# Optimization experiments

Hardware: AMD Instinct MI355X
Metric: run time of the kernel (lower is better)

Reference implementation:

```python
import jax, jax.numpy as jnp
import numpy as np

RES = 16          # grid resolution per axis -> num_models = 4096
L_XYZ = 10        # xyz positional-encoding frequencies -> input_ch = 63
L_DIR = 4         # dir positional-encoding frequencies -> input_ch_views = 27
W = 32
N_RAYS, N_SAMPLES = 1024, 128
NM = RES * RES * RES


def _embed(x, L):
    # NeRF frequency encoding: [x, sin(2^k x), cos(2^k x)] for k in 0..L-1
    freqs = 2.0 ** jnp.arange(L, dtype=x.dtype)          # (L,)
    xf = x[..., None, :] * freqs[:, None]                # (N, L, 3)
    enc = jnp.concatenate([jnp.sin(xf), jnp.cos(xf)], axis=-1)
    return jnp.concatenate([x, enc.reshape(x.shape[0], -1)], axis=-1)


def setup_inputs() -> dict:
    key = jax.random.key(0)
    ks = jax.random.split(key, 16)
    s = 0.05
    pts = jax.random.uniform(ks[0], (N_RAYS, N_SAMPLES, 3), dtype=jnp.float32)
    vd = jax.random.normal(ks[1], (N_RAYS, 3), dtype=jnp.float32)
    vd = vd / jnp.linalg.norm(vd, axis=-1, keepdims=True)
    return {
        "pts": pts,
        "viewdirs": vd,
        "pts_w0": s * jax.random.normal(ks[2], (NM, W, 63), dtype=jnp.float32),
        "pts_b0": s * jax.random.normal(ks[3], (NM, W), dtype=jnp.float32),
        "pts_w1": s * jax.random.normal(ks[4], (NM, W, W), dtype=jnp.float32),
        "pts_b1": s * jax.random.normal(ks[5], (NM, W), dtype=jnp.float32),
        "feat_w": s * jax.random.normal(ks[6], (NM, W, W), dtype=jnp.float32),
        "feat_b": s * jax.random.normal(ks[7], (NM, W), dtype=jnp.float32),
        "sigma_w": s * jax.random.normal(ks[8], (NM, 1, W), dtype=jnp.float32),
        "sigma_b": s * jax.random.normal(ks[9], (NM, 1), dtype=jnp.float32),
        "view_w": s * jax.random.normal(ks[10], (NM, W, W + 27), dtype=jnp.float32),
        "view_b": s * jax.random.normal(ks[11], (NM, W), dtype=jnp.float32),
        "rgb_w": s * jax.random.normal(ks[12], (NM, 3, W), dtype=jnp.float32),
        "rgb_b": s * jax.random.normal(ks[13], (NM, 3), dtype=jnp.float32),
    }


def reference(pts, viewdirs, pts_w0, pts_b0, pts_w1, pts_b1, feat_w, feat_b,
              sigma_w, sigma_b, view_w, view_b, rgb_w, rgb_b):
    n_rays, n_samples, _ = pts.shape
    p = pts.reshape(-1, 3)                                        # (N, 3)
    v = jnp.broadcast_to(viewdirs[:, None, :],
                         (n_rays, n_samples, 3)).reshape(-1, 3)   # (N, 3)

    # voxel index (aabb = [0,1]^3)
    scaled = jnp.clip(p * RES, 0.0, RES - 1.0)
    i3 = scaled.astype(jnp.int32)
    idx = i3[:, 0] * (RES * RES) + i3[:, 1] * RES + i3[:, 2]      # (N,)

    ep = _embed(p, L_XYZ)                                         # (N, 63)
    ev = _embed(v, L_DIR)                                         # (N, 27)

    # per-point tiny MLP with gathered weights: h @ w^T + b
    h = jax.nn.relu(jnp.einsum('nd,nod->no', ep, pts_w0[idx]) + pts_b0[idx])
    h = jax.nn.relu(jnp.einsum('nd,nod->no', h, pts_w1[idx]) + pts_b1[idx])

    sigma = jnp.einsum('nd,nod->no', h, sigma_w[idx]) + sigma_b[idx]   # (N, 1)
    feat = jnp.einsum('nd,nod->no', h, feat_w[idx]) + feat_b[idx]      # (N, W)

    h2 = jnp.concatenate([feat, ev], axis=-1)                          # (N, W+27)
    h2 = jax.nn.relu(jnp.einsum('nd,nod->no', h2, view_w[idx]) + view_b[idx])
    rgb = jnp.einsum('nd,nod->no', h2, rgb_w[idx]) + rgb_b[idx]        # (N, 3)

    out = jnp.concatenate([rgb, sigma], axis=-1).reshape(n_rays, n_samples, 4)
    return out[..., :3], out[..., 3:4]
```

## Files before the change

kernel.cpp:

```cpp
#include <hip/hip_runtime.h>

#define NM    4096
#define NPTS  131072
#define CAP   128

typedef _Float16 h8 __attribute__((ext_vector_type(8)));
typedef _Float16 h2 __attribute__((ext_vector_type(2)));
typedef float    f4 __attribute__((ext_vector_type(4)));
typedef int      i4 __attribute__((ext_vector_type(4)));

#define MF(a, b, c) __builtin_amdgcn_mfma_f32_16x16x32_f16((a), (b), (c), 0, 0, 0)

#if __has_builtin(__builtin_amdgcn_global_load_lds)
#define USE_DMA 1
#else
#define USE_DMA 0
#endif

static __device__ inline h2 pk(float a, float b) {
    return __builtin_bit_cast(h2, __builtin_amdgcn_cvt_pkrtz(a, b));
}

static __device__ inline h8 pack8(float u0, float u1, float u2, float u3,
                                  float u4, float u5, float u6, float u7) {
    i4 t;
    t[0] = __builtin_bit_cast(int, pk(u0, u1));
    t[1] = __builtin_bit_cast(int, pk(u2, u3));
    t[2] = __builtin_bit_cast(int, pk(u4, u5));
    t[3] = __builtin_bit_cast(int, pk(u6, u7));
    return __builtin_bit_cast(h8, t);
}

static __device__ inline h8 lds_row8(const float* __restrict__ X, int base,
                                     int d0, int lim) {
    float u[8];
    #pragma unroll
    for (int jj = 0; jj < 8; jj++) {
        int d = d0 + jj;
        float raw = X[base + d];
        u[jj] = (d < lim) ? raw : 0.f;
    }
    return pack8(u[0], u[1], u[2], u[3], u[4], u[5], u[6], u[7]);
}

static __device__ inline h8 lds_row8a(const float* __restrict__ X, int off) {
    f4 v0 = *(const f4*)(X + off);
    f4 v1 = *(const f4*)(X + off + 4);
    return pack8(v0[0], v0[1], v0[2], v0[3], v1[0], v1[1], v1[2], v1[3]);
}

static __device__ inline h8 load_row8(const float* __restrict__ rb, int d0, int lim) {
    float u[8];
    #pragma unroll
    for (int jj = 0; jj < 8; jj++) {
        int d = d0 + jj;
        u[jj] = (d < lim) ? rb[d] : 0.f;
    }
    return pack8(u[0], u[1], u[2], u[3], u[4], u[5], u[6], u[7]);
}

static __device__ inline float encdim(int d, int lim, float x, float y, float z) {
    int tt = d - 3;
    int k  = tt / 6;
    int r  = tt - 6 * k;
    float p = x;
    p = (r == 1 || r == 4) ? y : p;
    p = (r == 2 || r == 5) ? z : p;
    float f   = __int_as_float((k + 127) << 23);
    float arg = p * f + ((r >= 3) ? 1.57079632679f : 0.f);
    float sv  = __sinf(arg);
    float raw = (d == 0) ? x : ((d == 1) ? y : z);
    float val = (d < 3) ? raw : sv;
    return (d < lim) ? val : 0.f;
}

static __device__ inline h8 makeB(f4 d0, f4 d1, int quad, int col) {
    int laneA = ((quad & 1) * 2) * 16 + col;
    int laneB = laneA + 16;
    float a0 = __shfl(d0[0], laneA), b0 = __shfl(d1[0], laneA);
    float a1 = __shfl(d0[1], laneA), b1 = __shfl(d1[1], laneA);
    float a2 = __shfl(d0[2], laneA), b2 = __shfl(d1[2], laneA);
    float a3 = __shfl(d0[3], laneA), b3 = __shfl(d1[3], laneA);
    float a4 = __shfl(d0[0], laneB), b4 = __shfl(d1[0], laneB);
    float a5 = __shfl(d0[1], laneB), b5 = __shfl(d1[1], laneB);
    float a6 = __shfl(d0[2], laneB), b6 = __shfl(d1[2], laneB);
    float a7 = __shfl(d0[3], laneB), b7 = __shfl(d1[3], laneB);
    bool hi = quad >= 2;
    return pack8(hi ? b0 : a0, hi ? b1 : a1, hi ? b2 : a2, hi ? b3 : a3,
                 hi ? b4 : a4, hi ? b5 : a5, hi ? b6 : a6, hi ? b7 : a7);
}

static __device__ inline f4 relu4(f4 a) {
    f4 r;
    r[0] = fmaxf(a[0], 0.f); r[1] = fmaxf(a[1], 0.f);
    r[2] = fmaxf(a[2], 0.f); r[3] = fmaxf(a[3], 0.f);
    return r;
}

#if USE_DMA
static __device__ inline void dma16(const float* g, const float* l) {
    __builtin_amdgcn_global_load_lds(
        (const __attribute__((address_space(1))) void*)g,
        (__attribute__((address_space(3))) void*)l, 16, 0, 0);
}
#endif

__global__ __launch_bounds__(256) void k_bucket(const float* __restrict__ pts,
                                                int* __restrict__ count,
                                                int* __restrict__ plist) {
    int n = blockIdx.x * 256 + threadIdx.x;
    if (n >= NPTS) return;
    float x = pts[3 * n + 0], y = pts[3 * n + 1], z = pts[3 * n + 2];
    int ix = (int)fminf(fmaxf(x * 16.f, 0.f), 15.f);
    int iy = (int)fminf(fmaxf(y * 16.f, 0.f), 15.f);
    int iz = (int)fminf(fmaxf(z * 16.f, 0.f), 15.f);
    int v = (ix << 8) | (iy << 4) | iz;
    int pos = atomicAdd(&count[v], 1);
    if (pos < CAP) plist[v * CAP + pos] = n;
}

__global__ __launch_bounds__(64) void k_mlp(
    const float* __restrict__ pts, const float* __restrict__ vds,
    const float* __restrict__ w0g, const float* __restrict__ b0g,
    const float* __restrict__ w1g, const float* __restrict__ b1g,
    const float* __restrict__ fwg, const float* __restrict__ fbg,
    const float* __restrict__ swg, const float* __restrict__ sbg,
    const float* __restrict__ vwg, const float* __restrict__ vbg,
    const float* __restrict__ rwg, const float* __restrict__ rbg,
    const int* __restrict__ count, const int* __restrict__ plist,
    float* __restrict__ out) {
    __shared__ __align__(16) float X[3040];

    const int lane = threadIdx.x & 63;
    const int col  = lane & 15;
    const int quad = lane >> 4;
    const int k8   = quad * 8;
    const int v    = blockIdx.x;
    const int c    = min(count[v], CAP);
    if (c == 0) return;

#if USE_DMA
    {
        const float* g = w0g + (size_t)v * 2016;
        #pragma unroll
        for (int k = 0; k < 7; k++) dma16(g + k * 256 + lane * 4, X + k * 256);
        if (lane < 56) dma16(g + 1792 + lane * 4, X + 1792);
        const float* g1 = w1g + (size_t)v * 1024;
        #pragma unroll
        for (int k = 0; k < 4; k++) dma16(g1 + k * 256 + lane * 4, X + 2016 + k * 256);
    }
#endif

    const int prow0 = plist[v * CAP + lane];
    const int prow1 = plist[v * CAP + 64 + lane];
    auto chunk_idx = [&](int base) -> int {
        int e = min(base + col, c - 1);
        int a = __shfl(prow0, e);
        int b = __shfl(prow1, e - 64);
        return (e < 64) ? a : b;
    };

    f4 cB0[2], cB1[2], cFB[2], cVB[2];
    #pragma unroll
    for (int Ti = 0; Ti < 2; Ti++) {
        int ro = v * 32 + Ti * 16 + quad * 4;
        cB0[Ti] = *(const f4*)(b0g + ro);
        cB1[Ti] = *(const f4*)(b1g + ro);
        cFB[Ti] = *(const f4*)(fbg + ro);
        cVB[Ti] = *(const f4*)(vbg + ro);
    }
    const float rb0 = rbg[v * 3 + 0], rb1 = rbg[v * 3 + 1], rb2 = rbg[v * 3 + 2];
    const float sb  = sbg[v];

    int ncur = chunk_idx(0);
    float px = pts[3 * ncur], py = pts[3 * ncur + 1], pz = pts[3 * ncur + 2];
    int ray = ncur >> 7;
    float dx = vds[3 * ray], dy = vds[3 * ray + 1], dz = vds[3 * ray + 2];

    int nnxt = 0;
    float qx = 0.f, qy = 0.f, qz = 0.f, ex = 0.f, ey = 0.f, ez = 0.f;
    if (16 < c) {
        nnxt = chunk_idx(16);
        qx = pts[3 * nnxt]; qy = pts[3 * nnxt + 1]; qz = pts[3 * nnxt + 2];
        int r2 = nnxt >> 7;
        ex = vds[3 * r2]; ey = vds[3 * r2 + 1]; ez = vds[3 * r2 + 2];
    }

    h8 bE0, bE1, bD;
    auto encode = [&](float sx, float sy, float sz, float tx, float ty, float tz) {
        bE0 = pack8(encdim(k8 + 0, 63, sx, sy, sz), encdim(k8 + 1, 63, sx, sy, sz),
                    encdim(k8 + 2, 63, sx, sy, sz), encdim(k8 + 3, 63, sx, sy, sz),
                    encdim(k8 + 4, 63, sx, sy, sz), encdim(k8 + 5, 63, sx, sy, sz),
                    encdim(k8 + 6, 63, sx, sy, sz), encdim(k8 + 7, 63, sx, sy, sz));
        bE1 = pack8(encdim(32 + k8 + 0, 63, sx, sy, sz), encdim(32 + k8 + 1, 63, sx, sy, sz),
                    encdim(32 + k8 + 2, 63, sx, sy, sz), encdim(32 + k8 + 3, 63, sx, sy, sz),
                    encdim(32 + k8 + 4, 63, sx, sy, sz), encdim(32 + k8 + 5, 63, sx, sy, sz),
                    encdim(32 + k8 + 6, 63, sx, sy, sz), encdim(32 + k8 + 7, 63, sx, sy, sz));
        bD  = pack8(encdim(k8 + 0, 27, tx, ty, tz), encdim(k8 + 1, 27, tx, ty, tz),
                    encdim(k8 + 2, 27, tx, ty, tz), encdim(k8 + 3, 27, tx, ty, tz),
                    encdim(k8 + 4, 27, tx, ty, tz), encdim(k8 + 5, 27, tx, ty, tz),
                    encdim(k8 + 6, 27, tx, ty, tz), encdim(k8 + 7, 27, tx, ty, tz));
    };
    encode(px, py, pz, dx, dy, dz);

    h8 aW0[2][2], aW1[2], aVW[2][2], aFW[2], aSG, aRGB;

#if USE_DMA
    asm volatile("s_waitcnt vmcnt(0)" ::: "memory");
    __builtin_amdgcn_sched_barrier(0);
    #pragma unroll
    for (int Ti = 0; Ti < 2; Ti++) {
        int r0 = (Ti * 16 + col) * 63;
        aW0[Ti][0] = lds_row8(X, r0, k8, 63);
        aW0[Ti][1] = lds_row8(X, r0, 32 + k8, 63);
        aW1[Ti] = lds_row8a(X, 2016 + (Ti * 16 + col) * 32 + k8);
    }
    asm volatile("s_waitcnt lgkmcnt(0)" ::: "memory");
    __builtin_amdgcn_sched_barrier(0);

    {
        const float* g = vwg + (size_t)v * 1888;
        #pragma unroll
        for (int k = 0; k < 7; k++) dma16(g + k * 256 + lane * 4, X + k * 256);
        if (lane < 24) dma16(g + 1792 + lane * 4, X + 1792);
        const float* g1 = fwg + (size_t)v * 1024;
        #pragma unroll
        for (int k = 0; k < 4; k++) dma16(g1 + k * 256 + lane * 4, X + 1888 + k * 256);
        if (lane < 8)  dma16(swg + (size_t)v * 32 + lane * 4, X + 2912);
        if (lane < 24) dma16(rwg + (size_t)v * 96 + lane * 4, X + 2944);
    }
#else
    {
        #pragma unroll
        for (int Ti = 0; Ti < 2; Ti++) {
            const float* rb = w0g + (size_t)v * 2016 + (Ti * 16 + col) * 63;
            aW0[Ti][0] = load_row8(rb, k8, 63);
            aW0[Ti][1] = load_row8(rb, 32 + k8, 63);
            aW1[Ti] = load_row8(w1g + (size_t)v * 1024 + (Ti * 16 + col) * 32, k8, 32);
        }
    }
#endif

    const f4 z4 = {0.f, 0.f, 0.f, 0.f};

    f4 d0 = MF(aW0[0][0], bE0, cB0[0]); d0 = MF(aW0[0][1], bE1, d0);
    f4 d1 = MF(aW0[1][0], bE0, cB0[1]); d1 = MF(aW0[1][1], bE1, d1);
    d0 = relu4(d0); d1 = relu4(d1);
    h8 bH = makeB(d0, d1, quad, col);
    f4 e0 = MF(aW1[0], bH, cB1[0]);
    f4 e1 = MF(aW1[1], bH, cB1[1]);
    e0 = relu4(e0); e1 = relu4(e1);
    h8 bG = makeB(e0, e1, quad, col);

#if USE_DMA
    asm volatile("s_waitcnt vmcnt(0)" ::: "memory");
    __builtin_amdgcn_sched_barrier(0);
    #pragma unroll
    for (int Ti = 0; Ti < 2; Ti++) {
        int r1 = (Ti * 16 + col) * 59;
        aVW[Ti][0] = lds_row8(X, r1, k8, 59);
        aVW[Ti][1] = lds_row8(X, r1, 32 + k8, 59);
        aFW[Ti] = lds_row8a(X, 1888 + (Ti * 16 + col) * 32 + k8);
    }
    aSG  = (col == 0) ? lds_row8a(X, 2912 + k8) : h8{};
    aRGB = (col < 3) ? lds_row8a(X, 2944 + col * 32 + k8) : h8{};
#else
    {
        #pragma unroll
        for (int Ti = 0; Ti < 2; Ti++) {
            const float* rb = vwg + (size_t)v * 1888 + (Ti * 16 + col) * 59;
            aVW[Ti][0] = load_row8(rb, k8, 59);
            aVW[Ti][1] = load_row8(rb, 32 + k8, 59);
            aFW[Ti] = load_row8(fwg + (size_t)v * 1024 + (Ti * 16 + col) * 32, k8, 32);
        }
        aSG  = (col == 0) ? load_row8(swg + (size_t)v * 32, k8, 32) : h8{};
        aRGB = (col < 3) ? load_row8(rwg + (size_t)v * 96 + col * 32, k8, 32) : h8{};
    }
#endif

    {
        f4 s  = MF(aSG, bG, z4);
        f4 f0 = MF(aFW[0], bG, cFB[0]);
        f4 f1 = MF(aFW[1], bG, cFB[1]);
        h8 bF = makeB(f0, f1, quad, col);
        f4 v0 = MF(aVW[0][0], bF, cVB[0]); v0 = MF(aVW[0][1], bD, v0);
        f4 v1 = MF(aVW[1][0], bF, cVB[1]); v1 = MF(aVW[1][1], bD, v1);
        v0 = relu4(v0); v1 = relu4(v1);
        h8 bV = makeB(v0, v1, quad, col);
        f4 o  = MF(aRGB, bV, z4);
        if (quad == 0 && col < c) {
            out[3 * ncur + 0] = o[0] + rb0;
            out[3 * ncur + 1] = o[1] + rb1;
            out[3 * ncur + 2] = o[2] + rb2;
            out[3 * NPTS + ncur] = s[0] + sb;
        }
    }

    for (int base = 16; base < c; base += 16) {
        const int n = nnxt;
        const float cx = qx, cy = qy, cz = qz;
        const float fx = ex, fy = ey, fz = ez;

        if (base + 16 < c) {
            nnxt = chunk_idx(base + 16);
            qx = pts[3 * nnxt]; qy = pts[3 * nnxt + 1]; qz = pts[3 * nnxt + 2];
            int r2 = nnxt >> 7;
            ex = vds[3 * r2]; ey = vds[3 * r2 + 1]; ez = vds[3 * r2 + 2];
        }

        encode(cx, cy, cz, fx, fy, fz);

        d0 = MF(aW0[0][0], bE0, cB0[0]); d0 = MF(aW0[0][1], bE1, d0);
        d1 = MF(aW0[1][0], bE0, cB0[1]); d1 = MF(aW0[1][1], bE1, d1);
        d0 = relu4(d0); d1 = relu4(d1);
        bH = makeB(d0, d1, quad, col);

        e0 = MF(aW1[0], bH, cB1[0]);
        e1 = MF(aW1[1], bH, cB1[1]);
        e0 = relu4(e0); e1 = relu4(e1);
        bG = makeB(e0, e1, quad, col);

        f4 s  = MF(aSG, bG, z4);
        f4 f0 = MF(aFW[0], bG, cFB[0]);
        f4 f1 = MF(aFW[1], bG, cFB[1]);
        h8 bF = makeB(f0, f1, quad, col);

        f4 v0 = MF(aVW[0][0], bF, cVB[0]); v0 = MF(aVW[0][1], bD, v0);
        f4 v1 = MF(aVW[1][0], bF, cVB[1]); v1 = MF(aVW[1][1], bD, v1);
        v0 = relu4(v0); v1 = relu4(v1);
        h8 bV = makeB(v0, v1, quad, col);
        f4 o  = MF(aRGB, bV, z4);

        if (quad == 0 && (base + col) < c) {
            out[3 * n + 0] = o[0] + rb0;
            out[3 * n + 1] = o[1] + rb1;
            out[3 * n + 2] = o[2] + rb2;
            out[3 * NPTS + n] = s[0] + sb;
        }
    }
}

extern "C" void kernel_launch(void* const* d_in, const int* in_sizes, int n_in,
                              void* d_out, int out_size, void* d_ws, size_t ws_size,
                              hipStream_t stream) {
    const float* pts = (const float*)d_in[0];
    const float* vds = (const float*)d_in[1];
    const float* w0  = (const float*)d_in[2];
    const float* b0  = (const float*)d_in[3];
    const float* w1  = (const float*)d_in[4];
    const float* b1  = (const float*)d_in[5];
    const float* fw  = (const float*)d_in[6];
    const float* fb  = (const float*)d_in[7];
    const float* sw  = (const float*)d_in[8];
    const float* sb  = (const float*)d_in[9];
    const float* vw  = (const float*)d_in[10];
    const float* vb  = (const float*)d_in[11];
    const float* rw  = (const float*)d_in[12];
    const float* rb  = (const float*)d_in[13];
    float* out = (float*)d_out;

    int* count = (int*)d_ws;
    int* plist = (int*)((char*)d_ws + NM * sizeof(int));

    (void)hipMemsetAsync(count, 0, NM * sizeof(int), stream);
    k_bucket<<<NPTS / 256, 256, 0, stream>>>(pts, count, plist);
    k_mlp<<<NM, 64, 0, stream>>>(pts, vds, w0, b0, w1, b1, fw, fb, sw, sb,
                                 vw, vb, rw, rb, count, plist, out);
}
```

Measured before the change: 165.3 us.

## Process four voxels per block with double-buffered LDS weight prefetch

```diff
diff --git a/kernel.cpp b/kernel.cpp
--- a/kernel.cpp
+++ b/kernel.cpp
@@ -3,6 +3,8 @@
 #define NM    4096
 #define NPTS  131072
 #define CAP   128
+#define NV    4
+#define NBLK  (NM / NV)
 
 typedef _Float16 h8 __attribute__((ext_vector_type(8)));
 typedef _Float16 h2 __attribute__((ext_vector_type(2)));
@@ -129,64 +131,78 @@
     const float* __restrict__ rwg, const float* __restrict__ rbg,
     const int* __restrict__ count, const int* __restrict__ plist,
     float* __restrict__ out) {
-    __shared__ __align__(16) float X[3040];
+    __shared__ __align__(16) float X[2][3040];
 
     const int lane = threadIdx.x & 63;
     const int col  = lane & 15;
     const int quad = lane >> 4;
     const int k8   = quad * 8;
-    const int v    = blockIdx.x;
-    const int c    = min(count[v], CAP);
-    if (c == 0) return;
-
-#if USE_DMA
-    {
+    const int vbase = blockIdx.x * NV;
+
+#if USE_DMA
+    auto dmaA = [&](int v, float* Xb) {
         const float* g = w0g + (size_t)v * 2016;
         #pragma unroll
-        for (int k = 0; k < 7; k++) dma16(g + k * 256 + lane * 4, X + k * 256);
-        if (lane < 56) dma16(g + 1792 + lane * 4, X + 1792);
+        for (int k = 0; k < 7; k++) dma16(g + k * 256 + lane * 4, Xb + k * 256);
+        if (lane < 56) dma16(g + 1792 + lane * 4, Xb + 1792);
         const float* g1 = w1g + (size_t)v * 1024;
         #pragma unroll
-        for (int k = 0; k < 4; k++) dma16(g1 + k * 256 + lane * 4, X + 2016 + k * 256);
-    }
-#endif
-
-    const int prow0 = plist[v * CAP + lane];
-    const int prow1 = plist[v * CAP + 64 + lane];
-    auto chunk_idx = [&](int base) -> int {
-        int e = min(base + col, c - 1);
-        int a = __shfl(prow0, e);
-        int b = __shfl(prow1, e - 64);
-        return (e < 64) ? a : b;
+        for (int k = 0; k < 4; k++) dma16(g1 + k * 256 + lane * 4, Xb + 2016 + k * 256);
     };
-
-    f4 cB0[2], cB1[2], cFB[2], cVB[2];
-    #pragma unroll
-    for (int Ti = 0; Ti < 2; Ti++) {
-        int ro = v * 32 + Ti * 16 + quad * 4;
-        cB0[Ti] = *(const f4*)(b0g + ro);
-        cB1[Ti] = *(const f4*)(b1g + ro);
-        cFB[Ti] = *(const f4*)(fbg + ro);
-        cVB[Ti] = *(const f4*)(vbg + ro);
-    }
-    const float rb0 = rbg[v * 3 + 0], rb1 = rbg[v * 3 + 1], rb2 = rbg[v * 3 + 2];
-    const float sb  = sbg[v];
-
-    int ncur = chunk_idx(0);
-    float px = pts[3 * ncur], py = pts[3 * ncur + 1], pz = pts[3 * ncur + 2];
-    int ray = ncur >> 7;
-    float dx = vds[3 * ray], dy = vds[3 * ray + 1], dz = vds[3 * ray + 2];
-
-    int nnxt = 0;
-    float qx = 0.f, qy = 0.f, qz = 0.f, ex = 0.f, ey = 0.f, ez = 0.f;
-    if (16 < c) {
-        nnxt = chunk_idx(16);
-        qx = pts[3 * nnxt]; qy = pts[3 * nnxt + 1]; qz = pts[3 * nnxt + 2];
-        int r2 = nnxt >> 7;
-        ex = vds[3 * r2]; ey = vds[3 * r2 + 1]; ez = vds[3 * r2 + 2];
-    }
-
+    auto dmaB = [&](int v, float* Xb) {
+        const float* g = vwg + (size_t)v * 1888;
+        #pragma unroll
+        for (int k = 0; k < 7; k++) dma16(g + k * 256 + lane * 4, Xb + k * 256);
+        if (lane < 24) dma16(g + 1792 + lane * 4, Xb + 1792);
+        const float* g1 = fwg + (size_t)v * 1024;
+        #pragma unroll
+        for (int k = 0; k < 4; k++) dma16(g1 + k * 256 + lane * 4, Xb + 1888 + k * 256);
+        if (lane < 8)  dma16(swg + (size_t)v * 32 + lane * 4, Xb + 2912);
+        if (lane < 24) dma16(rwg + (size_t)v * 96 + lane * 4, Xb + 2944);
+    };
+#endif
+
+    int c_n = 0, prow0_n = 0, prow1_n = 0;
+    f4 cB0_n[2], cB1_n[2], cFB_n[2], cVB_n[2];
+    float rb0_n = 0.f, rb1_n = 0.f, rb2_n = 0.f, sb_n = 0.f;
+    int n0_n = 0;
+    float px_n = 0.f, py_n = 0.f, pz_n = 0.f, dx_n = 0.f, dy_n = 0.f, dz_n = 0.f;
+
+    auto pf_meta = [&](int v) {
+        c_n = min(count[v], CAP);
+        prow0_n = plist[v * CAP + lane];
+        prow1_n = plist[v * CAP + 64 + lane];
+        #pragma unroll
+        for (int Ti = 0; Ti < 2; Ti++) {
+            int ro = v * 32 + Ti * 16 + quad * 4;
+            cB0_n[Ti] = *(const f4*)(b0g + ro);
+            cB1_n[Ti] = *(const f4*)(b1g + ro);
+            cFB_n[Ti] = *(const f4*)(fbg + ro);
+            cVB_n[Ti] = *(const f4*)(vbg + ro);
+        }
+        rb0_n = rbg[v * 3 + 0]; rb1_n = rbg[v * 3 + 1]; rb2_n = rbg[v * 3 + 2];
+        sb_n  = sbg[v];
+    };
+    auto pf_pts = [&]() {
+        if (c_n > 0) {
+            int e = min(col, c_n - 1);
+            n0_n = __shfl(prow0_n, e);
+            px_n = pts[3 * n0_n]; py_n = pts[3 * n0_n + 1]; pz_n = pts[3 * n0_n + 2];
+            int ray = n0_n >> 7;
+            dx_n = vds[3 * ray]; dy_n = vds[3 * ray + 1]; dz_n = vds[3 * ray + 2];
+        }
+    };
+
+    pf_meta(vbase);
+#if USE_DMA
+    dmaA(vbase, X[0]);
+#endif
+    pf_pts();
+
+    h8 aW0[2][2], aW1[2], aVW[2][2], aFW[2], aSG, aRGB;
     h8 bE0, bE1, bD;
+    const f4 z4 = {0.f, 0.f, 0.f, 0.f};
+
     auto encode = [&](float sx, float sy, float sz, float tx, float ty, float tz) {
         bE0 = pack8(encdim(k8 + 0, 63, sx, sy, sz), encdim(k8 + 1, 63, sx, sy, sz),
                     encdim(k8 + 2, 63, sx, sy, sz), encdim(k8 + 3, 63, sx, sy, sz),
@@ -201,142 +217,182 @@
                     encdim(k8 + 4, 27, tx, ty, tz), encdim(k8 + 5, 27, tx, ty, tz),
                     encdim(k8 + 6, 27, tx, ty, tz), encdim(k8 + 7, 27, tx, ty, tz));
     };
-    encode(px, py, pz, dx, dy, dz);
-
-    h8 aW0[2][2], aW1[2], aVW[2][2], aFW[2], aSG, aRGB;
-
-#if USE_DMA
-    asm volatile("s_waitcnt vmcnt(0)" ::: "memory");
-    __builtin_amdgcn_sched_barrier(0);
-    #pragma unroll
-    for (int Ti = 0; Ti < 2; Ti++) {
-        int r0 = (Ti * 16 + col) * 63;
-        aW0[Ti][0] = lds_row8(X, r0, k8, 63);
-        aW0[Ti][1] = lds_row8(X, r0, 32 + k8, 63);
-        aW1[Ti] = lds_row8a(X, 2016 + (Ti * 16 + col) * 32 + k8);
-    }
-    asm volatile("s_waitcnt lgkmcnt(0)" ::: "memory");
-    __builtin_amdgcn_sched_barrier(0);
-
-    {
-        const float* g = vwg + (size_t)v * 1888;
-        #pragma unroll
-        for (int k = 0; k < 7; k++) dma16(g + k * 256 + lane * 4, X + k * 256);
-        if (lane < 24) dma16(g + 1792 + lane * 4, X + 1792);
-        const float* g1 = fwg + (size_t)v * 1024;
-        #pragma unroll
-        for (int k = 0; k < 4; k++) dma16(g1 + k * 256 + lane * 4, X + 1888 + k * 256);
-        if (lane < 8)  dma16(swg + (size_t)v * 32 + lane * 4, X + 2912);
-        if (lane < 24) dma16(rwg + (size_t)v * 96 + lane * 4, X + 2944);
-    }
+
+    int cur = 0;
+    for (int iv = 0; iv < NV; iv++) {
+        float* Xb = X[cur];
+        const int v = vbase + iv;
+
+        const int c = c_n;
+        const int prow0 = prow0_n, prow1 = prow1_n;
+        f4 cB0[2] = {cB0_n[0], cB0_n[1]}, cB1[2] = {cB1_n[0], cB1_n[1]};
+        f4 cFB[2] = {cFB_n[0], cFB_n[1]}, cVB[2] = {cVB_n[0], cVB_n[1]};
+        const float rb0 = rb0_n, rb1 = rb1_n, rb2 = rb2_n, sb = sb_n;
+        const int n0 = n0_n;
+        const float px = px_n, py = py_n, pz = pz_n;
+        const float dx = dx_n, dy = dy_n, dz = dz_n;
+        const bool hasW = c > 0;
+
+        auto chunk_idx = [&](int base) -> int {
+            int e = min(base + col, c - 1);
+            int a = __shfl(prow0, e);
+            int b = __shfl(prow1, e - 64);
+            return (e < 64) ? a : b;
+        };
+
+#if USE_DMA
+        asm volatile("s_waitcnt vmcnt(0)" ::: "memory");
+        __builtin_amdgcn_sched_barrier(0);
+
+        if (hasW) {
+            #pragma unroll
+            for (int Ti = 0; Ti < 2; Ti++) {
+                int r0 = (Ti * 16 + col) * 63;
+                aW0[Ti][0] = lds_row8(Xb, r0, k8, 63);
+                aW0[Ti][1] = lds_row8(Xb, r0, 32 + k8, 63);
+                aW1[Ti] = lds_row8a(Xb, 2016 + (Ti * 16 + col) * 32 + k8);
+            }
+        }
 #else
-    {
-        #pragma unroll
-        for (int Ti = 0; Ti < 2; Ti++) {
-            const float* rb = w0g + (size_t)v * 2016 + (Ti * 16 + col) * 63;
-            aW0[Ti][0] = load_row8(rb, k8, 63);
-            aW0[Ti][1] = load_row8(rb, 32 + k8, 63);
-            aW1[Ti] = load_row8(w1g + (size_t)v * 1024 + (Ti * 16 + col) * 32, k8, 32);
-        }
-    }
-#endif
-
-    const f4 z4 = {0.f, 0.f, 0.f, 0.f};
-
-    f4 d0 = MF(aW0[0][0], bE0, cB0[0]); d0 = MF(aW0[0][1], bE1, d0);
-    f4 d1 = MF(aW0[1][0], bE0, cB0[1]); d1 = MF(aW0[1][1], bE1, d1);
-    d0 = relu4(d0); d1 = relu4(d1);
-    h8 bH = makeB(d0, d1, quad, col);
-    f4 e0 = MF(aW1[0], bH, cB1[0]);
-    f4 e1 = MF(aW1[1], bH, cB1[1]);
-    e0 = relu4(e0); e1 = relu4(e1);
-    h8 bG = makeB(e0, e1, quad, col);
-
-#if USE_DMA
-    asm volatile("s_waitcnt vmcnt(0)" ::: "memory");
-    __builtin_amdgcn_sched_barrier(0);
-    #pragma unroll
-    for (int Ti = 0; Ti < 2; Ti++) {
-        int r1 = (Ti * 16 + col) * 59;
-        aVW[Ti][0] = lds_row8(X, r1, k8, 59);
-        aVW[Ti][1] = lds_row8(X, r1, 32 + k8, 59);
-        aFW[Ti] = lds_row8a(X, 1888 + (Ti * 16 + col) * 32 + k8);
-    }
-    aSG  = (col == 0) ? lds_row8a(X, 2912 + k8) : h8{};
-    aRGB = (col < 3) ? lds_row8a(X, 2944 + col * 32 + k8) : h8{};
+        if (hasW) {
+            #pragma unroll
+            for (int Ti = 0; Ti < 2; Ti++) {
+                const float* rb = w0g + (size_t)v * 2016 + (Ti * 16 + col) * 63;
+                aW0[Ti][0] = load_row8(rb, k8, 63);
+                aW0[Ti][1] = load_row8(rb, 32 + k8, 63);
+                aW1[Ti] = load_row8(w1g + (size_t)v * 1024 + (Ti * 16 + col) * 32, k8, 32);
+            }
+        }
+#endif
+
+        int n1 = 0;
+        float qx = 0.f, qy = 0.f, qz = 0.f, ex = 0.f, ey = 0.f, ez = 0.f;
+        if (c > 16) {
+            n1 = chunk_idx(16);
+            qx = pts[3 * n1]; qy = pts[3 * n1 + 1]; qz = pts[3 * n1 + 2];
+            int r2 = n1 >> 7;
+            ex = vds[3 * r2]; ey = vds[3 * r2 + 1]; ez = vds[3 * r2 + 2];
+        }
+
+        if (iv + 1 < NV) pf_meta(v + 1);
+
+#if USE_DMA
+        asm volatile("s_waitcnt lgkmcnt(0)" ::: "memory");
+        __builtin_amdgcn_sched_barrier(0);
+        dmaB(v, Xb);
+#endif
+
+        f4 d0, d1, e0, e1;
+        h8 bH, bG;
+        if (hasW) {
+            encode(px, py, pz, dx, dy, dz);
+            d0 = MF(aW0[0][0], bE0, cB0[0]); d0 = MF(aW0[0][1], bE1, d0);
+            d1 = MF(aW0[1][0], bE0, cB0[1]); d1 = MF(aW0[1][1], bE1, d1);
+            d0 = relu4(d0); d1 = relu4(d1);
+            bH = makeB(d0, d1, quad, col);
+            e0 = MF(aW1[0], bH, cB1[0]);
+            e1 = MF(aW1[1], bH, cB1[1]);
+            e0 = relu4(e0); e1 = relu4(e1);
+            bG = makeB(e0, e1, quad, col);
+        }
+
+#if USE_DMA
+        __builtin_amdgcn_sched_barrier(0);
+        asm volatile("s_waitcnt vmcnt(0)" ::: "memory");
+        __builtin_amdgcn_sched_barrier(0);
+
+        if (hasW) {
+            #pragma unroll
+            for (int Ti = 0; Ti < 2; Ti++) {
+                int r1 = (Ti * 16 + col) * 59;
+                aVW[Ti][0] = lds_row8(Xb, r1, k8, 59);
+                aVW[Ti][1] = lds_row8(Xb, r1, 32 + k8, 59);
+                aFW[Ti] = lds_row8a(Xb, 1888 + (Ti * 16 + col) * 32 + k8);
+            }
+            aSG  = (col == 0) ? lds_row8a(Xb, 2912 + k8) : h8{};
+            aRGB = (col < 3) ? lds_row8a(Xb, 2944 + col * 32 + k8) : h8{};
+        }
 #else
-    {
-        #pragma unroll
-        for (int Ti = 0; Ti < 2; Ti++) {
-            const float* rb = vwg + (size_t)v * 1888 + (Ti * 16 + col) * 59;
-            aVW[Ti][0] = load_row8(rb, k8, 59);
-            aVW[Ti][1] = load_row8(rb, 32 + k8, 59);
-            aFW[Ti] = load_row8(fwg + (size_t)v * 1024 + (Ti * 16 + col) * 32, k8, 32);
-        }
-        aSG  = (col == 0) ? load_row8(swg + (size_t)v * 32, k8, 32) : h8{};
-        aRGB = (col < 3) ? load_row8(rwg + (size_t)v * 96 + col * 32, k8, 32) : h8{};
-    }
-#endif
-
-    {
-        f4 s  = MF(aSG, bG, z4);
-        f4 f0 = MF(aFW[0], bG, cFB[0]);
-        f4 f1 = MF(aFW[1], bG, cFB[1]);
-        h8 bF = makeB(f0, f1, quad, col);
-        f4 v0 = MF(aVW[0][0], bF, cVB[0]); v0 = MF(aVW[0][1], bD, v0);
-        f4 v1 = MF(aVW[1][0], bF, cVB[1]); v1 = MF(aVW[1][1], bD, v1);
-        v0 = relu4(v0); v1 = relu4(v1);
-        h8 bV = makeB(v0, v1, quad, col);
-        f4 o  = MF(aRGB, bV, z4);
-        if (quad == 0 && col < c) {
-            out[3 * ncur + 0] = o[0] + rb0;
-            out[3 * ncur + 1] = o[1] + rb1;
-            out[3 * ncur + 2] = o[2] + rb2;
-            out[3 * NPTS + ncur] = s[0] + sb;
-        }
-    }
-
-    for (int base = 16; base < c; base += 16) {
-        const int n = nnxt;
-        const float cx = qx, cy = qy, cz = qz;
-        const float fx = ex, fy = ey, fz = ez;
-
-        if (base + 16 < c) {
-            nnxt = chunk_idx(base + 16);
-            qx = pts[3 * nnxt]; qy = pts[3 * nnxt + 1]; qz = pts[3 * nnxt + 2];
-            int r2 = nnxt >> 7;
-            ex = vds[3 * r2]; ey = vds[3 * r2 + 1]; ez = vds[3 * r2 + 2];
-        }
-
-        encode(cx, cy, cz, fx, fy, fz);
-
-        d0 = MF(aW0[0][0], bE0, cB0[0]); d0 = MF(aW0[0][1], bE1, d0);
-        d1 = MF(aW0[1][0], bE0, cB0[1]); d1 = MF(aW0[1][1], bE1, d1);
-        d0 = relu4(d0); d1 = relu4(d1);
-        bH = makeB(d0, d1, quad, col);
-
-        e0 = MF(aW1[0], bH, cB1[0]);
-        e1 = MF(aW1[1], bH, cB1[1]);
-        e0 = relu4(e0); e1 = relu4(e1);
-        bG = makeB(e0, e1, quad, col);
-
-        f4 s  = MF(aSG, bG, z4);
-        f4 f0 = MF(aFW[0], bG, cFB[0]);
-        f4 f1 = MF(aFW[1], bG, cFB[1]);
-        h8 bF = makeB(f0, f1, quad, col);
-
-        f4 v0 = MF(aVW[0][0], bF, cVB[0]); v0 = MF(aVW[0][1], bD, v0);
-        f4 v1 = MF(aVW[1][0], bF, cVB[1]); v1 = MF(aVW[1][1], bD, v1);
-        v0 = relu4(v0); v1 = relu4(v1);
-        h8 bV = makeB(v0, v1, quad, col);
-        f4 o  = MF(aRGB, bV, z4);
-
-        if (quad == 0 && (base + col) < c) {
-            out[3 * n + 0] = o[0] + rb0;
-            out[3 * n + 1] = o[1] + rb1;
-            out[3 * n + 2] = o[2] + rb2;
-            out[3 * NPTS + n] = s[0] + sb;
-        }
+        if (hasW) {
+            #pragma unroll
+            for (int Ti = 0; Ti < 2; Ti++) {
+                const float* rb = vwg + (size_t)v * 1888 + (Ti * 16 + col) * 59;
+                aVW[Ti][0] = load_row8(rb, k8, 59);
+                aVW[Ti][1] = load_row8(rb, 32 + k8, 59);
+                aFW[Ti] = load_row8(fwg + (size_t)v * 1024 + (Ti * 16 + col) * 32, k8, 32);
+            }
+            aSG  = (col == 0) ? load_row8(swg + (size_t)v * 32, k8, 32) : h8{};
+            aRGB = (col < 3) ? load_row8(rwg + (size_t)v * 96 + col * 32, k8, 32) : h8{};
+        }
+#endif
+
+        if (iv + 1 < NV) {
+            pf_pts();
+#if USE_DMA
+            dmaA(v + 1, X[cur ^ 1]);
+#endif
+        }
+
+        if (hasW) {
+            {
+                f4 s  = MF(aSG, bG, z4);
+                f4 f0 = MF(aFW[0], bG, cFB[0]);
+                f4 f1 = MF(aFW[1], bG, cFB[1]);
+                h8 bF = makeB(f0, f1, quad, col);
+                f4 v0 = MF(aVW[0][0], bF, cVB[0]); v0 = MF(aVW[0][1], bD, v0);
+                f4 v1 = MF(aVW[1][0], bF, cVB[1]); v1 = MF(aVW[1][1], bD, v1);
+                v0 = relu4(v0); v1 = relu4(v1);
+                h8 bV = makeB(v0, v1, quad, col);
+                f4 o  = MF(aRGB, bV, z4);
+                if (quad == 0 && col < c) {
+                    out[3 * n0 + 0] = o[0] + rb0;
+                    out[3 * n0 + 1] = o[1] + rb1;
+                    out[3 * n0 + 2] = o[2] + rb2;
+                    out[3 * NPTS + n0] = s[0] + sb;
+                }
+            }
+
+            auto do_chunk = [&](int n, bool active) {
+                d0 = MF(aW0[0][0], bE0, cB0[0]); d0 = MF(aW0[0][1], bE1, d0);
+                d1 = MF(aW0[1][0], bE0, cB0[1]); d1 = MF(aW0[1][1], bE1, d1);
+                d0 = relu4(d0); d1 = relu4(d1);
+                bH = makeB(d0, d1, quad, col);
+                e0 = MF(aW1[0], bH, cB1[0]);
+                e1 = MF(aW1[1], bH, cB1[1]);
+                e0 = relu4(e0); e1 = relu4(e1);
+                bG = makeB(e0, e1, quad, col);
+                f4 s  = MF(aSG, bG, z4);
+                f4 f0 = MF(aFW[0], bG, cFB[0]);
+                f4 f1 = MF(aFW[1], bG, cFB[1]);
+                h8 bF = makeB(f0, f1, quad, col);
+                f4 v0 = MF(aVW[0][0], bF, cVB[0]); v0 = MF(aVW[0][1], bD, v0);
+                f4 v1 = MF(aVW[1][0], bF, cVB[1]); v1 = MF(aVW[1][1], bD, v1);
+                v0 = relu4(v0); v1 = relu4(v1);
+                h8 bV = makeB(v0, v1, quad, col);
+                f4 o  = MF(aRGB, bV, z4);
+                if (quad == 0 && active) {
+                    out[3 * n + 0] = o[0] + rb0;
+                    out[3 * n + 1] = o[1] + rb1;
+                    out[3 * n + 2] = o[2] + rb2;
+                    out[3 * NPTS + n] = s[0] + sb;
+                }
+            };
+
+            if (c > 16) {
+                encode(qx, qy, qz, ex, ey, ez);
+                do_chunk(n1, (16 + col) < c);
+            }
+            for (int base = 32; base < c; base += 16) {
+                int n = chunk_idx(base);
+                float gx = pts[3 * n], gy = pts[3 * n + 1], gz = pts[3 * n + 2];
+                int r3 = n >> 7;
+                float hx = vds[3 * r3], hy = vds[3 * r3 + 1], hz = vds[3 * r3 + 2];
+                encode(gx, gy, gz, hx, hy, hz);
+                do_chunk(n, (base + col) < c);
+            }
+        }
+
+        cur ^= 1;
     }
 }
 
@@ -364,6 +420,6 @@
 
     (void)hipMemsetAsync(count, 0, NM * sizeof(int), stream);
     k_bucket<<<NPTS / 256, 256, 0, stream>>>(pts, count, plist);
-    k_mlp<<<NM, 64, 0, stream>>>(pts, vds, w0, b0, w1, b1, fw, fb, sw, sb,
-                                 vw, vb, rw, rb, count, plist, out);
-}
+    k_mlp<<<NBLK, 64, 0, stream>>>(pts, vds, w0, b0, w1, b1, fw, fb, sw, sb,
+                                   vw, vb, rw, rb, count, plist, out);
+}
```

Measured after the change: 170.0 us. 1.03x slower.

## Replace LDS DMA staging with direct vectorized global weight loads into registers

Applied to the files above, without the earlier changes.

```diff
diff --git a/kernel.cpp b/kernel.cpp
--- a/kernel.cpp
+++ b/kernel.cpp
@@ -8,14 +8,9 @@
 typedef _Float16 h2 __attribute__((ext_vector_type(2)));
 typedef float    f4 __attribute__((ext_vector_type(4)));
 typedef int      i4 __attribute__((ext_vector_type(4)));
+typedef float    f4u __attribute__((ext_vector_type(4), aligned(4)));
 
 #define MF(a, b, c) __builtin_amdgcn_mfma_f32_16x16x32_f16((a), (b), (c), 0, 0, 0)
-
-#if __has_builtin(__builtin_amdgcn_global_load_lds)
-#define USE_DMA 1
-#else
-#define USE_DMA 0
-#endif
 
 static __device__ inline h2 pk(float a, float b) {
     return __builtin_bit_cast(h2, __builtin_amdgcn_cvt_pkrtz(a, b));
@@ -29,34 +24,6 @@
     t[2] = __builtin_bit_cast(int, pk(u4, u5));
     t[3] = __builtin_bit_cast(int, pk(u6, u7));
     return __builtin_bit_cast(h8, t);
-}
-
-static __device__ inline h8 lds_row8(const float* __restrict__ X, int base,
-                                     int d0, int lim) {
-    float u[8];
-    #pragma unroll
-    for (int jj = 0; jj < 8; jj++) {
-        int d = d0 + jj;
-        float raw = X[base + d];
-        u[jj] = (d < lim) ? raw : 0.f;
-    }
-    return pack8(u[0], u[1], u[2], u[3], u[4], u[5], u[6], u[7]);
-}
-
-static __device__ inline h8 lds_row8a(const float* __restrict__ X, int off) {
-    f4 v0 = *(const f4*)(X + off);
-    f4 v1 = *(const f4*)(X + off + 4);
-    return pack8(v0[0], v0[1], v0[2], v0[3], v1[0], v1[1], v1[2], v1[3]);
-}
-
-static __device__ inline h8 load_row8(const float* __restrict__ rb, int d0, int lim) {
-    float u[8];
-    #pragma unroll
-    for (int jj = 0; jj < 8; jj++) {
-        int d = d0 + jj;
-        u[jj] = (d < lim) ? rb[d] : 0.f;
-    }
-    return pack8(u[0], u[1], u[2], u[3], u[4], u[5], u[6], u[7]);
 }
 
 static __device__ inline float encdim(int d, int lim, float x, float y, float z) {
@@ -97,14 +64,6 @@
     return r;
 }
 
-#if USE_DMA
-static __device__ inline void dma16(const float* g, const float* l) {
-    __builtin_amdgcn_global_load_lds(
-        (const __attribute__((address_space(1))) void*)g,
-        (__attribute__((address_space(3))) void*)l, 16, 0, 0);
-}
-#endif
-
 __global__ __launch_bounds__(256) void k_bucket(const float* __restrict__ pts,
                                                 int* __restrict__ count,
                                                 int* __restrict__ plist) {
@@ -119,7 +78,7 @@
     if (pos < CAP) plist[v * CAP + pos] = n;
 }
 
-__global__ __launch_bounds__(64) void k_mlp(
+__global__ __launch_bounds__(64, 3) void k_mlp(
     const float* __restrict__ pts, const float* __restrict__ vds,
     const float* __restrict__ w0g, const float* __restrict__ b0g,
     const float* __restrict__ w1g, const float* __restrict__ b1g,
@@ -129,8 +88,6 @@
     const float* __restrict__ rwg, const float* __restrict__ rbg,
     const int* __restrict__ count, const int* __restrict__ plist,
     float* __restrict__ out) {
-    __shared__ __align__(16) float X[3040];
-
     const int lane = threadIdx.x & 63;
     const int col  = lane & 15;
     const int quad = lane >> 4;
@@ -138,18 +95,6 @@
     const int v    = blockIdx.x;
     const int c    = min(count[v], CAP);
     if (c == 0) return;
-
-#if USE_DMA
-    {
-        const float* g = w0g + (size_t)v * 2016;
-        #pragma unroll
-        for (int k = 0; k < 7; k++) dma16(g + k * 256 + lane * 4, X + k * 256);
-        if (lane < 56) dma16(g + 1792 + lane * 4, X + 1792);
-        const float* g1 = w1g + (size_t)v * 1024;
-        #pragma unroll
-        for (int k = 0; k < 4; k++) dma16(g1 + k * 256 + lane * 4, X + 2016 + k * 256);
-    }
-#endif
 
     const int prow0 = plist[v * CAP + lane];
     const int prow1 = plist[v * CAP + 64 + lane];
@@ -160,6 +105,85 @@
         return (e < 64) ? a : b;
     };
 
+    h8 aW0[2][2], aW1[2], aVW[2][2], aFW[2], aSG, aRGB;
+    const bool q3 = (k8 == 24);
+    #pragma unroll
+    for (int Ti = 0; Ti < 2; Ti++) {
+        const bool rare = (v == NM - 1) && (Ti == 1) && (col == 15) && q3;
+
+        const float* r0 = w0g + (size_t)v * 2016 + (Ti * 16 + col) * 63;
+        {
+            f4u a = *(const f4u*)(r0 + k8);
+            f4u b = *(const f4u*)(r0 + k8 + 4);
+            aW0[Ti][0] = pack8(a[0], a[1], a[2], a[3], b[0], b[1], b[2], b[3]);
+        }
+        if (rare) {
+            float u[8];
+            #pragma unroll
+            for (int j = 0; j < 8; j++) {
+                int d = 32 + k8 + j;
+                u[j] = (d < 63) ? r0[min(d, 62)] : 0.f;
+            }
+            aW0[Ti][1] = pack8(u[0], u[1], u[2], u[3], u[4], u[5], u[6], u[7]);
+        } else {
+            f4u a = *(const f4u*)(r0 + 32 + k8);
+            f4u b = *(const f4u*)(r0 + 36 + k8);
+            float u7 = q3 ? 0.f : b[3];
+            aW0[Ti][1] = pack8(a[0], a[1], a[2], a[3], b[0], b[1], b[2], u7);
+        }
+
+        const float* r1 = vwg + (size_t)v * 1888 + (Ti * 16 + col) * 59;
+        {
+            f4u a = *(const f4u*)(r1 + k8);
+            f4u b = *(const f4u*)(r1 + k8 + 4);
+            aVW[Ti][0] = pack8(a[0], a[1], a[2], a[3], b[0], b[1], b[2], b[3]);
+        }
+        if (rare) {
+            float u[8];
+            #pragma unroll
+            for (int j = 0; j < 8; j++) {
+                int d = 32 + k8 + j;
+                u[j] = (d < 59) ? r1[min(d, 58)] : 0.f;
+            }
+            aVW[Ti][1] = pack8(u[0], u[1], u[2], u[3], u[4], u[5], u[6], u[7]);
+        } else {
+            f4u a = *(const f4u*)(r1 + 32 + k8);
+            f4u b = *(const f4u*)(r1 + 36 + k8);
+            float u3 = q3 ? 0.f : a[3];
+            float u4 = q3 ? 0.f : b[0];
+            float u5 = q3 ? 0.f : b[1];
+            float u6 = q3 ? 0.f : b[2];
+            float u7 = q3 ? 0.f : b[3];
+            aVW[Ti][1] = pack8(a[0], a[1], a[2], u3, u4, u5, u6, u7);
+        }
+
+        {
+            const float* r2 = w1g + (size_t)v * 1024 + (Ti * 16 + col) * 32 + k8;
+            f4 a = *(const f4*)r2;
+            f4 b = *(const f4*)(r2 + 4);
+            aW1[Ti] = pack8(a[0], a[1], a[2], a[3], b[0], b[1], b[2], b[3]);
+        }
+        {
+            const float* r3 = fwg + (size_t)v * 1024 + (Ti * 16 + col) * 32 + k8;
+            f4 a = *(const f4*)r3;
+            f4 b = *(const f4*)(r3 + 4);
+            aFW[Ti] = pack8(a[0], a[1], a[2], a[3], b[0], b[1], b[2], b[3]);
+        }
+    }
+    {
+        const float* rs = swg + (size_t)v * 32 + k8;
+        f4 a = *(const f4*)rs;
+        f4 b = *(const f4*)(rs + 4);
+        aSG = (col == 0) ? pack8(a[0], a[1], a[2], a[3], b[0], b[1], b[2], b[3]) : h8{};
+    }
+    {
+        int cc = min(col, 2);
+        const float* rr = rwg + (size_t)v * 96 + cc * 32 + k8;
+        f4 a = *(const f4*)rr;
+        f4 b = *(const f4*)(rr + 4);
+        aRGB = (col < 3) ? pack8(a[0], a[1], a[2], a[3], b[0], b[1], b[2], b[3]) : h8{};
+    }
+
     f4 cB0[2], cB1[2], cFB[2], cVB[2];
     #pragma unroll
     for (int Ti = 0; Ti < 2; Ti++) {
@@ -172,20 +196,7 @@
     const float rb0 = rbg[v * 3 + 0], rb1 = rbg[v * 3 + 1], rb2 = rbg[v * 3 + 2];
     const float sb  = sbg[v];
 
-    int ncur = chunk_idx(0);
-    float px = pts[3 * ncur], py = pts[3 * ncur + 1], pz = pts[3 * ncur + 2];
-    int ray = ncur >> 7;
-    float dx = vds[3 * ray], dy = vds[3 * ray + 1], dz = vds[3 * ray + 2];
-
-    int nnxt = 0;
-    float qx = 0.f, qy = 0.f, qz = 0.f, ex = 0.f, ey = 0.f, ez = 0.f;
-    if (16 < c) {
-        nnxt = chunk_idx(16);
-        qx = pts[3 * nnxt]; qy = pts[3 * nnxt + 1]; qz = pts[3 * nnxt + 2];
-        int r2 = nnxt >> 7;
-        ex = vds[3 * r2]; ey = vds[3 * r2 + 1]; ez = vds[3 * r2 + 2];
-    }
-
+    const f4 z4 = {0.f, 0.f, 0.f, 0.f};
     h8 bE0, bE1, bD;
     auto encode = [&](float sx, float sy, float sz, float tx, float ty, float tz) {
         bE0 = pack8(encdim(k8 + 0, 63, sx, sy, sz), encdim(k8 + 1, 63, sx, sy, sz),
@@ -201,84 +212,16 @@
                     encdim(k8 + 4, 27, tx, ty, tz), encdim(k8 + 5, 27, tx, ty, tz),
                     encdim(k8 + 6, 27, tx, ty, tz), encdim(k8 + 7, 27, tx, ty, tz));
     };
-    encode(px, py, pz, dx, dy, dz);
-
-    h8 aW0[2][2], aW1[2], aVW[2][2], aFW[2], aSG, aRGB;
-
-#if USE_DMA
-    asm volatile("s_waitcnt vmcnt(0)" ::: "memory");
-    __builtin_amdgcn_sched_barrier(0);
-    #pragma unroll
-    for (int Ti = 0; Ti < 2; Ti++) {
-        int r0 = (Ti * 16 + col) * 63;
-        aW0[Ti][0] = lds_row8(X, r0, k8, 63);
-        aW0[Ti][1] = lds_row8(X, r0, 32 + k8, 63);
-        aW1[Ti] = lds_row8a(X, 2016 + (Ti * 16 + col) * 32 + k8);
-    }
-    asm volatile("s_waitcnt lgkmcnt(0)" ::: "memory");
-    __builtin_amdgcn_sched_barrier(0);
-
-    {
-        const float* g = vwg + (size_t)v * 1888;
-        #pragma unroll
-        for (int k = 0; k < 7; k++) dma16(g + k * 256 + lane * 4, X + k * 256);
-        if (lane < 24) dma16(g + 1792 + lane * 4, X + 1792);
-        const float* g1 = fwg + (size_t)v * 1024;
-        #pragma unroll
-        for (int k = 0; k < 4; k++) dma16(g1 + k * 256 + lane * 4, X + 1888 + k * 256);
-        if (lane < 8)  dma16(swg + (size_t)v * 32 + lane * 4, X + 2912);
-        if (lane < 24) dma16(rwg + (size_t)v * 96 + lane * 4, X + 2944);
-    }
-#else
-    {
-        #pragma unroll
-        for (int Ti = 0; Ti < 2; Ti++) {
-            const float* rb = w0g + (size_t)v * 2016 + (Ti * 16 + col) * 63;
-            aW0[Ti][0] = load_row8(rb, k8, 63);
-            aW0[Ti][1] = load_row8(rb, 32 + k8, 63);
-            aW1[Ti] = load_row8(w1g + (size_t)v * 1024 + (Ti * 16 + col) * 32, k8, 32);
-        }
-    }
-#endif
-
-    const f4 z4 = {0.f, 0.f, 0.f, 0.f};
-
-    f4 d0 = MF(aW0[0][0], bE0, cB0[0]); d0 = MF(aW0[0][1], bE1, d0);
-    f4 d1 = MF(aW0[1][0], bE0, cB0[1]); d1 = MF(aW0[1][1], bE1, d1);
-    d0 = relu4(d0); d1 = relu4(d1);
-    h8 bH = makeB(d0, d1, quad, col);
-    f4 e0 = MF(aW1[0], bH, cB1[0]);
-    f4 e1 = MF(aW1[1], bH, cB1[1]);
-    e0 = relu4(e0); e1 = relu4(e1);
-    h8 bG = makeB(e0, e1, quad, col);
-
-#if USE_DMA
-    asm volatile("s_waitcnt vmcnt(0)" ::: "memory");
-    __builtin_amdgcn_sched_barrier(0);
-    #pragma unroll
-    for (int Ti = 0; Ti < 2; Ti++) {
-        int r1 = (Ti * 16 + col) * 59;
-        aVW[Ti][0] = lds_row8(X, r1, k8, 59);
-        aVW[Ti][1] = lds_row8(X, r1, 32 + k8, 59);
-        aFW[Ti] = lds_row8a(X, 1888 + (Ti * 16 + col) * 32 + k8);
-    }
-    aSG  = (col == 0) ? lds_row8a(X, 2912 + k8) : h8{};
-    aRGB = (col < 3) ? lds_row8a(X, 2944 + col * 32 + k8) : h8{};
-#else
-    {
-        #pragma unroll
-        for (int Ti = 0; Ti < 2; Ti++) {
-            const float* rb = vwg + (size_t)v * 1888 + (Ti * 16 + col) * 59;
-            aVW[Ti][0] = load_row8(rb, k8, 59);
-            aVW[Ti][1] = load_row8(rb, 32 + k8, 59);
-            aFW[Ti] = load_row8(fwg + (size_t)v * 1024 + (Ti * 16 + col) * 32, k8, 32);
-        }
-        aSG  = (col == 0) ? load_row8(swg + (size_t)v * 32, k8, 32) : h8{};
-        aRGB = (col < 3) ? load_row8(rwg + (size_t)v * 96 + col * 32, k8, 32) : h8{};
-    }
-#endif
-
-    {
+
+    auto do_chunk = [&](int n, bool active) {
+        f4 d0 = MF(aW0[0][0], bE0, cB0[0]); d0 = MF(aW0[0][1], bE1, d0);
+        f4 d1 = MF(aW0[1][0], bE0, cB0[1]); d1 = MF(aW0[1][1], bE1, d1);
+        d0 = relu4(d0); d1 = relu4(d1);
+        h8 bH = makeB(d0, d1, quad, col);
+        f4 e0 = MF(aW1[0], bH, cB1[0]);
+        f4 e1 = MF(aW1[1], bH, cB1[1]);
+        e0 = relu4(e0); e1 = relu4(e1);
+        h8 bG = makeB(e0, e1, quad, col);
         f4 s  = MF(aSG, bG, z4);
         f4 f0 = MF(aFW[0], bG, cFB[0]);
         f4 f1 = MF(aFW[1], bG, cFB[1]);
@@ -288,13 +231,30 @@
         v0 = relu4(v0); v1 = relu4(v1);
         h8 bV = makeB(v0, v1, quad, col);
         f4 o  = MF(aRGB, bV, z4);
-        if (quad == 0 && col < c) {
-            out[3 * ncur + 0] = o[0] + rb0;
-            out[3 * ncur + 1] = o[1] + rb1;
-            out[3 * ncur + 2] = o[2] + rb2;
-            out[3 * NPTS + ncur] = s[0] + sb;
-        }
-    }
+        if (quad == 0 && active) {
+            out[3 * n + 0] = o[0] + rb0;
+            out[3 * n + 1] = o[1] + rb1;
+            out[3 * n + 2] = o[2] + rb2;
+            out[3 * NPTS + n] = s[0] + sb;
+        }
+    };
+
+    int ncur = chunk_idx(0);
+    float px = pts[3 * ncur], py = pts[3 * ncur + 1], pz = pts[3 * ncur + 2];
+    int ray = ncur >> 7;
+    float dx = vds[3 * ray], dy = vds[3 * ray + 1], dz = vds[3 * ray + 2];
+
+    int nnxt = 0;
+    float qx = 0.f, qy = 0.f, qz = 0.f, ex = 0.f, ey = 0.f, ez = 0.f;
+    if (16 < c) {
+        nnxt = chunk_idx(16);
+        qx = pts[3 * nnxt]; qy = pts[3 * nnxt + 1]; qz = pts[3 * nnxt + 2];
+        int r2 = nnxt >> 7;
+        ex = vds[3 * r2]; ey = vds[3 * r2 + 1]; ez = vds[3 * r2 + 2];
+    }
+
+    encode(px, py, pz, dx, dy, dz);
+    do_chunk(ncur, col < c);
 
     for (int base = 16; base < c; base += 16) {
         const int n = nnxt;
@@ -309,34 +269,7 @@
         }
 
         encode(cx, cy, cz, fx, fy, fz);
-
-        d0 = MF(aW0[0][0], bE0, cB0[0]); d0 = MF(aW0[0][1], bE1, d0);
-        d1 = MF(aW0[1][0], bE0, cB0[1]); d1 = MF(aW0[1][1], bE1, d1);
-        d0 = relu4(d0); d1 = relu4(d1);
-        bH = makeB(d0, d1, quad, col);
-
-        e0 = MF(aW1[0], bH, cB1[0]);
-        e1 = MF(aW1[1], bH, cB1[1]);
-        e0 = relu4(e0); e1 = relu4(e1);
-        bG = makeB(e0, e1, quad, col);
-
-        f4 s  = MF(aSG, bG, z4);
-        f4 f0 = MF(aFW[0], bG, cFB[0]);
-        f4 f1 = MF(aFW[1], bG, cFB[1]);
-        h8 bF = makeB(f0, f1, quad, col);
-
-        f4 v0 = MF(aVW[0][0], bF, cVB[0]); v0 = MF(aVW[0][1], bD, v0);
-        f4 v1 = MF(aVW[1][0], bF, cVB[1]); v1 = MF(aVW[1][1], bD, v1);
-        v0 = relu4(v0); v1 = relu4(v1);
-        h8 bV = makeB(v0, v1, quad, col);
-        f4 o  = MF(aRGB, bV, z4);
-
-        if (quad == 0 && (base + col) < c) {
-            out[3 * n + 0] = o[0] + rb0;
-            out[3 * n + 1] = o[1] + rb1;
-            out[3 * n + 2] = o[2] + rb2;
-            out[3 * NPTS + n] = s[0] + sb;
-        }
+        do_chunk(n, (base + col) < c);
     }
 }
 
```

New measurement: 170.8 us. 3.3% more time.
